# Kernel tuning notes

Hardware: AMD Instinct MI355X
Metric: run time of the kernel (lower is better)

Reference implementation:

```python
import jax, jax.numpy as jnp
import numpy as np

NEG_SLOPE = 0.01  # nn.LeakyReLU default


def setup_inputs() -> dict:
    key = jax.random.key(0)
    k1, k2, k3, k4, k5, k6 = jax.random.split(key, 6)
    N, E, F_IN, F_OUT = 50000, 800000, 256, 64
    x = jax.random.normal(k1, (N, F_IN), dtype=jnp.float32)
    src = jax.random.randint(k2, (E,), 0, N, dtype=jnp.int32)
    dst = jax.random.randint(k3, (E,), 0, N, dtype=jnp.int32)
    # nn.init.normal_(weight, 0, 0.5) for both Linear layers (no bias)
    W1 = 0.5 * jax.random.normal(k4, (F_OUT, F_IN), dtype=jnp.float32)
    W2 = 0.5 * jax.random.normal(k5, (F_OUT, F_OUT), dtype=jnp.float32)
    # detGAT.a = torch.rand(2*out_feats, 1)
    a = jax.random.uniform(k6, (2 * F_OUT, 1), dtype=jnp.float32)
    return {"x": x, "W1": W1, "W2": W2, "a": a, "src": src, "dst": dst}


def reference(x, W1, W2, a, src, dst):
    N, d = x.shape[0], W1.shape[0]
    # model_base: linear -> (dropout, identity in eval) -> relu, twice
    z = jax.nn.relu(x @ W1.T)
    h = jax.nn.relu(z @ W2.T)  # [N, d]
    # detGAT edge score: LeakyReLU(concat([h_dst, h_src]) @ a)
    # split a so we compute per-node dot products once instead of an [E, 2d] concat
    a_dst, a_src = a[:d, 0], a[d:, 0]
    s_dst = h @ a_dst  # [N]
    s_src = h @ a_src  # [N]
    score = jax.nn.leaky_relu(s_dst[dst] + s_src[src], NEG_SLOPE)  # [E]
    # edge_softmax: softmax over incoming edges of each destination node
    m = jax.ops.segment_max(score, dst, num_segments=N)  # [N]
    e = jnp.exp(score - m[dst])
    ssum = jax.ops.segment_sum(e, dst, num_segments=N)  # [N]
    w = e / ssum[dst]  # [E]
    # weighted scatter-sum of src features to dst nodes
    res = jax.ops.segment_sum(h[src] * w[:, None], dst, num_segments=N)  # [N, d]
    return jax.nn.relu(h - res)
```

## Files before the change

kernel.cpp:

```cpp
#include <hip/hip_runtime.h>
#include <math.h>

#define F_IN 256
#define F_OUT 64
#define NEG_SLOPE 0.01f
#define CAP 8192
#define NB2 256

typedef unsigned short ushort8_t __attribute__((ext_vector_type(8)));
typedef __bf16 bf16x8 __attribute__((ext_vector_type(8)));
typedef float f32x16 __attribute__((ext_vector_type(16)));

__device__ inline unsigned short f2bf(float f) {
    unsigned u = __float_as_uint(f);
    u += 0x7FFF + ((u >> 16) & 1);
    return (unsigned short)(u >> 16);
}
__device__ inline float bf2f(unsigned short u) {
    return __uint_as_float(((unsigned)u) << 16);
}
__device__ inline void splitbf(float x, unsigned short& hi, unsigned short& lo) {
    hi = f2bf(x);
    lo = f2bf(x - bf2f(hi));
}
__device__ inline bf16x8 asbf8(ushort8_t u) {
    union { ushort8_t u; bf16x8 b; } c; c.u = u; return c.b;
}
__device__ inline void split8(const float4& p0, const float4& p1, bf16x8& ah, bf16x8& al) {
    ushort8_t h, l;
    unsigned short th, tl;
    splitbf(p0.x, th, tl); h[0] = th; l[0] = tl;
    splitbf(p0.y, th, tl); h[1] = th; l[1] = tl;
    splitbf(p0.z, th, tl); h[2] = th; l[2] = tl;
    splitbf(p0.w, th, tl); h[3] = th; l[3] = tl;
    splitbf(p1.x, th, tl); h[4] = th; l[4] = tl;
    splitbf(p1.y, th, tl); h[5] = th; l[5] = tl;
    splitbf(p1.z, th, tl); h[6] = th; l[6] = tl;
    splitbf(p1.w, th, tl); h[7] = th; l[7] = tl;
    ah = asbf8(h); al = asbf8(l);
}
__device__ inline float redq32(float v) {
    v += __shfl_xor(v, 1);  v += __shfl_xor(v, 2);  v += __shfl_xor(v, 4);
    v += __shfl_xor(v, 8);  v += __shfl_xor(v, 16);
    return v;
}

__global__ __launch_bounds__(256)
void prep_frag_kernel(const float* __restrict__ W1, const float* __restrict__ W2,
                      unsigned short* __restrict__ w1fh, unsigned short* __restrict__ w1fl,
                      unsigned short* __restrict__ w2fh, unsigned short* __restrict__ w2fl)
{
    int idx = blockIdx.x * blockDim.x + threadIdx.x;
    int jj = idx & 7, l = (idx >> 3) & 63, t = idx >> 9;
    {
        int nt = t & 1, gks = t >> 1;
        int f = nt * 32 + (l & 31);
        int k = gks * 16 + (l >> 5) * 8 + jj;
        unsigned short hi, lo;
        splitbf(W1[f * F_IN + k], hi, lo);
        w1fh[idx] = hi; w1fl[idx] = lo;
    }
    if (idx < 4096) {
        int nt = t & 1, ks = t >> 1;
        int f = nt * 32 + (l & 31);
        int j = ks * 16 + (l >> 5) * 8 + jj;
        unsigned short hi, lo;
        splitbf(W2[f * F_OUT + j], hi, lo);
        w2fh[idx] = hi; w2fl[idx] = lo;
    }
}

__global__ __launch_bounds__(128, 2)
void mlp_kernel(const float* __restrict__ x,
                const unsigned short* __restrict__ w1fh,
                const unsigned short* __restrict__ w1fl,
                const unsigned short* __restrict__ w2fh,
                const unsigned short* __restrict__ w2fl,
                const float* __restrict__ a,
                unsigned short* __restrict__ hb,
                float* __restrict__ sdst,
                float* __restrict__ ssrc, int N)
{
    __shared__ __align__(16) unsigned short zbuf[2 * 4224];

    const int tid = threadIdx.x;
    const int lane = tid & 63;
    const int w = __builtin_amdgcn_readfirstlane(tid >> 6);
    const int ml = lane & 31;
    const int q = lane >> 5;
    const int node0w = blockIdx.x * 64 + w * 32;

    unsigned short* zh = zbuf + w * 4224;
    unsigned short* zl = zh + 2112;

    const int rowc = min(node0w + ml, N - 1);
    const float* __restrict__ xrow = x + (size_t)rowc * F_IN + q * 8;

    f32x16 acc0, acc1;
#pragma unroll
    for (int i = 0; i < 16; i++) { acc0[i] = 0.f; acc1[i] = 0.f; }

    float4 p0 = *(const float4*)(xrow);
    float4 p1 = *(const float4*)(xrow + 4);
    ushort8_t b0h = *(const ushort8_t*)(w1fh + (lane) * 8);
    ushort8_t b0l = *(const ushort8_t*)(w1fl + (lane) * 8);
    ushort8_t b1h = *(const ushort8_t*)(w1fh + (64 + lane) * 8);
    ushort8_t b1l = *(const ushort8_t*)(w1fl + (64 + lane) * 8);

#pragma unroll
    for (int gks = 0; gks < 16; gks++) {
        const int nx = gks < 15 ? gks + 1 : 15;
        float4 q0 = *(const float4*)(xrow + nx * 16);
        float4 q1 = *(const float4*)(xrow + nx * 16 + 4);
        ushort8_t c0h = *(const ushort8_t*)(w1fh + ((nx * 2 + 0) * 64 + lane) * 8);
        ushort8_t c0l = *(const ushort8_t*)(w1fl + ((nx * 2 + 0) * 64 + lane) * 8);
        ushort8_t c1h = *(const ushort8_t*)(w1fh + ((nx * 2 + 1) * 64 + lane) * 8);
        ushort8_t c1l = *(const ushort8_t*)(w1fl + ((nx * 2 + 1) * 64 + lane) * 8);

        bf16x8 ah, al;
        split8(p0, p1, ah, al);
        acc0 = __builtin_amdgcn_mfma_f32_32x32x16_bf16(ah, asbf8(b0h), acc0, 0, 0, 0);
        acc0 = __builtin_amdgcn_mfma_f32_32x32x16_bf16(ah, asbf8(b0l), acc0, 0, 0, 0);
        acc0 = __builtin_amdgcn_mfma_f32_32x32x16_bf16(al, asbf8(b0h), acc0, 0, 0, 0);
        acc1 = __builtin_amdgcn_mfma_f32_32x32x16_bf16(ah, asbf8(b1h), acc1, 0, 0, 0);
        acc1 = __builtin_amdgcn_mfma_f32_32x32x16_bf16(ah, asbf8(b1l), acc1, 0, 0, 0);
        acc1 = __builtin_amdgcn_mfma_f32_32x32x16_bf16(al, asbf8(b1h), acc1, 0, 0, 0);

        p0 = q0; p1 = q1;
        b0h = c0h; b0l = c0l; b1h = c1h; b1l = c1l;
    }

#pragma unroll
    for (int reg = 0; reg < 16; reg++) {
        int nd = (reg & 3) + 8 * (reg >> 2) + 4 * q;
        float z0 = fmaxf(acc0[reg], 0.f);
        float z1 = fmaxf(acc1[reg], 0.f);
        unsigned short h_, l_;
        splitbf(z0, h_, l_);
        zh[nd * 66 + ml] = h_; zl[nd * 66 + ml] = l_;
        splitbf(z1, h_, l_);
        zh[nd * 66 + 32 + ml] = h_; zl[nd * 66 + 32 + ml] = l_;
    }

    f32x16 hacc0, hacc1;
#pragma unroll
    for (int i = 0; i < 16; i++) { hacc0[i] = 0.f; hacc1[i] = 0.f; }
#pragma unroll
    for (int ks = 0; ks < 4; ks++) {
        ushort8_t wh0 = *(const ushort8_t*)(w2fh + ((ks * 2 + 0) * 64 + lane) * 8);
        ushort8_t wl0 = *(const ushort8_t*)(w2fl + ((ks * 2 + 0) * 64 + lane) * 8);
        ushort8_t wh1 = *(const ushort8_t*)(w2fh + ((ks * 2 + 1) * 64 + lane) * 8);
        ushort8_t wl1 = *(const ushort8_t*)(w2fl + ((ks * 2 + 1) * 64 + lane) * 8);
        bf16x8 ah = asbf8(*(const ushort8_t*)(zh + ml * 66 + ks * 16 + q * 8));
        bf16x8 al = asbf8(*(const ushort8_t*)(zl + ml * 66 + ks * 16 + q * 8));
        hacc0 = __builtin_amdgcn_mfma_f32_32x32x16_bf16(ah, asbf8(wh0), hacc0, 0, 0, 0);
        hacc0 = __builtin_amdgcn_mfma_f32_32x32x16_bf16(ah, asbf8(wl0), hacc0, 0, 0, 0);
        hacc0 = __builtin_amdgcn_mfma_f32_32x32x16_bf16(al, asbf8(wh0), hacc0, 0, 0, 0);
        hacc1 = __builtin_amdgcn_mfma_f32_32x32x16_bf16(ah, asbf8(wh1), hacc1, 0, 0, 0);
        hacc1 = __builtin_amdgcn_mfma_f32_32x32x16_bf16(ah, asbf8(wl1), hacc1, 0, 0, 0);
        hacc1 = __builtin_amdgcn_mfma_f32_32x32x16_bf16(al, asbf8(wh1), hacc1, 0, 0, 0);
    }

    const float aD0 = a[ml],            aD1 = a[32 + ml];
    const float aS0 = a[F_OUT + ml],    aS1 = a[F_OUT + 32 + ml];

    float sdv = 0.f, ssv = 0.f;
#pragma unroll
    for (int reg = 0; reg < 16; reg++) {
        int nd = (reg & 3) + 8 * (reg >> 2) + 4 * q;
        float h0 = fmaxf(hacc0[reg], 0.f);
        float h1 = fmaxf(hacc1[reg], 0.f);
        float td = redq32(h0 * aD0 + h1 * aD1);
        float ts = redq32(h0 * aS0 + h1 * aS1);
        if (ml == nd) { sdv = td; ssv = ts; }
        int gn = node0w + nd;
        if (gn < N) {
            hb[(size_t)gn * F_OUT + ml]      = f2bf(h0);
            hb[(size_t)gn * F_OUT + 32 + ml] = f2bf(h1);
        }
    }
    {
        int gn = node0w + ml;
        if ((((ml >> 2) & 1) == q) && gn < N) {
            sdst[gn] = sdv;
            ssrc[gn] = ssv;
        }
    }
}

__global__ __launch_bounds__(1024)
void scatter_fused_kernel(const int* __restrict__ src, const int* __restrict__ dst,
                          int* __restrict__ cursor, int* __restrict__ edata,
                          int E, int chunk)
{
    __shared__ int lh[256], lbase[256], lcur[256];
    const int tid = threadIdx.x;
    if (tid < 256) lh[tid] = 0;
    __syncthreads();
    const int beg = blockIdx.x * chunk;
    const int end = min(E, beg + chunk);
    for (int i = beg + tid; i < end; i += 1024)
        atomicAdd(&lh[((unsigned)dst[i]) >> 8], 1);
    __syncthreads();
    if (tid < 256) {
        int c = lh[tid];
        lbase[tid] = c ? atomicAdd(&cursor[tid], c) : 0;
        lcur[tid] = 0;
    }
    __syncthreads();
    for (int i = beg + tid; i < end; i += 1024) {
        int d = dst[i];
        int s = src[i];
        int b = ((unsigned)d) >> 8;
        int rk = atomicAdd(&lcur[b], 1);
        edata[b * CAP + lbase[b] + rk] = ((d & 0xFF) << 16) | s;
    }
}

__global__ __launch_bounds__(1024)
void bucket_sort_kernel(const int* __restrict__ cursor,
                        const int* __restrict__ edata,
                        int* __restrict__ ssorted,
                        int* __restrict__ cnt, int* __restrict__ offs, int N)
{
    __shared__ int hist[256];
    __shared__ int excl[256];
    const int tid = threadIdx.x;
    const int lane = tid & 63;
    const int cb = blockIdx.x;
    const int base = cb * CAP;
    const int ecnt = cursor[cb];

    if (tid < 256) hist[tid] = 0;
    __syncthreads();
    for (int i = tid; i < ecnt; i += 1024)
        atomicAdd(&hist[((unsigned)edata[base + i]) >> 16], 1);
    __syncthreads();

    if (tid < 64) {
        int v0 = hist[lane * 4], v1 = hist[lane * 4 + 1];
        int v2 = hist[lane * 4 + 2], v3 = hist[lane * 4 + 3];
        int ts = v0 + v1 + v2 + v3;
        int s = ts;
#pragma unroll
        for (int d = 1; d < 64; d <<= 1) {
            int t = __shfl_up(s, d);
            if (lane >= d) s += t;
        }
        int e = s - ts;
        excl[lane * 4] = e;
        excl[lane * 4 + 1] = e + v0;
        excl[lane * 4 + 2] = e + v0 + v1;
        excl[lane * 4 + 3] = e + v0 + v1 + v2;
    }
    __syncthreads();

    if (tid < 256) {
        int d = cb * 256 + tid;
        if (d < N) {
            cnt[d] = hist[tid];
            offs[d] = base + excl[tid];
        }
    }
    __syncthreads();

    for (int i = tid; i < ecnt; i += 1024) {
        int pack = edata[base + i];
        int low = ((unsigned)pack) >> 16;
        int rk = atomicAdd(&excl[low], 1);
        ssorted[base + rk] = pack & 0xFFFF;
    }
}

__global__ __launch_bounds__(256)
void aggregate_kernel(const unsigned short* __restrict__ hb,
                      const float* __restrict__ sdst,
                      const float* __restrict__ ssrc,
                      const int* __restrict__ offs,
                      const int* __restrict__ cnt,
                      const int* __restrict__ ssorted,
                      float* __restrict__ out, int N)
{
    __shared__ float2 ws_sh[4][64];
    const int lane = threadIdx.x & 63;
    const int wid = threadIdx.x >> 6;
    const int d = blockIdx.x * 4 + wid;
    if (d >= N) return;

    const int off = offs[d];
    const int deg = cnt[d];
    const float sdd = sdst[d];
    float M = -INFINITY, S = 0.f, res = 0.f;

    for (int cb = 0; cb < deg; cb += 64) {
        int ce = min(64, deg - cb);
        float score = -INFINITY;
        int s = 0;
        if (lane < ce) {
            s = ssorted[off + cb + lane];
            float sc = sdd + ssrc[s];
            score = sc > 0.f ? sc : NEG_SLOPE * sc;
        }
        float mc = score;
#pragma unroll
        for (int dd = 32; dd > 0; dd >>= 1)
            mc = fmaxf(mc, __shfl_xor(mc, dd));
        float newM = fmaxf(M, mc);
        float scale = __expf(M - newM);
        float w = (lane < ce) ? __expf(score - newM) : 0.f;
        ws_sh[wid][lane] = make_float2(w, __int_as_float(s));
        float csum = w;
#pragma unroll
        for (int dd = 32; dd > 0; dd >>= 1)
            csum += __shfl_xor(csum, dd);
        S = S * scale + csum;
        __builtin_amdgcn_wave_barrier();

        float c[8];
#pragma unroll
        for (int i = 0; i < 8; i++) c[i] = 0.f;
        const int ceo = (ce + 7) & ~7;
        for (int e = 0; e < ceo; e += 8) {
#pragma unroll
            for (int i = 0; i < 8; i++) {
                float2 t = ws_sh[wid][e + i];
                int se = __builtin_amdgcn_readfirstlane(__float_as_int(t.y));
                c[i] = fmaf(t.x, bf2f(hb[((unsigned)se << 6) + lane]), c[i]);
            }
        }
        float t = ((c[0] + c[1]) + (c[2] + c[3])) + ((c[4] + c[5]) + (c[6] + c[7]));
        res = res * scale + t;
        __builtin_amdgcn_wave_barrier();
        M = newM;
    }

    float hf = bf2f(hb[((unsigned)d << 6) + lane]);
    float r = (S > 0.f) ? (hf - res / S) : hf;
    out[(size_t)d * F_OUT + lane] = r > 0.f ? r : 0.f;
}

extern "C" void kernel_launch(void* const* d_in, const int* in_sizes, int n_in,
                              void* d_out, int out_size, void* d_ws,
                              size_t ws_size, hipStream_t stream)
{
    const float* x  = (const float*)d_in[0];
    const float* W1 = (const float*)d_in[1];
    const float* W2 = (const float*)d_in[2];
    const float* a  = (const float*)d_in[3];
    const int* src  = (const int*)d_in[4];
    const int* dst  = (const int*)d_in[5];
    const int N = in_sizes[0] / F_IN;
    const int E = in_sizes[4];

    float* ws = (float*)d_ws;
    float* sdst = ws;
    float* ssrc = sdst + N;
    unsigned short* w1fh = (unsigned short*)(ssrc + N);
    unsigned short* w1fl = w1fh + 16384;
    unsigned short* w2fh = w1fl + 16384;
    unsigned short* w2fl = w2fh + 4096;
    unsigned short* hb = w2fl + 4096;
    int* cnt    = (int*)(hb + (size_t)N * F_OUT);
    int* offs   = cnt + N;
    int* cursor = offs + N;
    int* edata  = cursor + 256;
    int* ssorted = edata + 196 * CAP;

    const int nbc = (N + 255) >> 8;
    const int chunk = (E + NB2 - 1) / NB2;

    hipMemsetAsync(cursor, 0, 256 * sizeof(int), stream);
    prep_frag_kernel<<<64, 256, 0, stream>>>(W1, W2, w1fh, w1fl, w2fh, w2fl);
    mlp_kernel<<<(N + 63) / 64, 128, 0, stream>>>(x, w1fh, w1fl, w2fh, w2fl, a,
                                                  hb, sdst, ssrc, N);
    scatter_fused_kernel<<<NB2, 1024, 0, stream>>>(src, dst, cursor, edata, E, chunk);
    bucket_sort_kernel<<<nbc, 1024, 0, stream>>>(cursor, edata, ssorted, cnt, offs, N);
    aggregate_kernel<<<(N + 3) / 4, 256, 0, stream>>>(hb, sdst, ssrc, offs, cnt,
                                                      ssorted, (float*)d_out, N);
}
```

Measured before the change: 164.3 us.

## Merge independent stages into shared launches to cut kernel count

The weight-fragment prep now runs inside the edge-scatter kernel as 16 extra blocks, and the MLP and per-bucket sort run as disjoint block ranges of one launch. Five kernels become three, which removes launch gaps and lets the compute-heavy MLP overlap with the memory and atomic-bound sort. The MLP blocks grow to 256 threads (4 waves) so both roles share a block size, and the sort now runs with 256 threads instead of 1024. That lowers sort parallelism per bucket and raises LDS use per block, which may cut occupancy for the MLP part.

Result: faster. 152.9 us (-7.0%).

```diff
diff --git a/kernel.cpp b/kernel.cpp
--- a/kernel.cpp
+++ b/kernel.cpp
@@ -45,159 +45,43 @@
     return v;
 }
 
-__global__ __launch_bounds__(256)
-void prep_frag_kernel(const float* __restrict__ W1, const float* __restrict__ W2,
-                      unsigned short* __restrict__ w1fh, unsigned short* __restrict__ w1fl,
-                      unsigned short* __restrict__ w2fh, unsigned short* __restrict__ w2fl)
-{
-    int idx = blockIdx.x * blockDim.x + threadIdx.x;
-    int jj = idx & 7, l = (idx >> 3) & 63, t = idx >> 9;
-    {
-        int nt = t & 1, gks = t >> 1;
-        int f = nt * 32 + (l & 31);
-        int k = gks * 16 + (l >> 5) * 8 + jj;
-        unsigned short hi, lo;
-        splitbf(W1[f * F_IN + k], hi, lo);
-        w1fh[idx] = hi; w1fl[idx] = lo;
-    }
-    if (idx < 4096) {
-        int nt = t & 1, ks = t >> 1;
-        int f = nt * 32 + (l & 31);
-        int j = ks * 16 + (l >> 5) * 8 + jj;
-        unsigned short hi, lo;
-        splitbf(W2[f * F_OUT + j], hi, lo);
-        w2fh[idx] = hi; w2fl[idx] = lo;
-    }
-}
-
-__global__ __launch_bounds__(128, 2)
-void mlp_kernel(const float* __restrict__ x,
-                const unsigned short* __restrict__ w1fh,
-                const unsigned short* __restrict__ w1fl,
-                const unsigned short* __restrict__ w2fh,
-                const unsigned short* __restrict__ w2fl,
-                const float* __restrict__ a,
-                unsigned short* __restrict__ hb,
-                float* __restrict__ sdst,
-                float* __restrict__ ssrc, int N)
-{
-    __shared__ __align__(16) unsigned short zbuf[2 * 4224];
-
-    const int tid = threadIdx.x;
-    const int lane = tid & 63;
-    const int w = __builtin_amdgcn_readfirstlane(tid >> 6);
-    const int ml = lane & 31;
-    const int q = lane >> 5;
-    const int node0w = blockIdx.x * 64 + w * 32;
-
-    unsigned short* zh = zbuf + w * 4224;
-    unsigned short* zl = zh + 2112;
-
-    const int rowc = min(node0w + ml, N - 1);
-    const float* __restrict__ xrow = x + (size_t)rowc * F_IN + q * 8;
-
-    f32x16 acc0, acc1;
-#pragma unroll
-    for (int i = 0; i < 16; i++) { acc0[i] = 0.f; acc1[i] = 0.f; }
-
-    float4 p0 = *(const float4*)(xrow);
-    float4 p1 = *(const float4*)(xrow + 4);
-    ushort8_t b0h = *(const ushort8_t*)(w1fh + (lane) * 8);
-    ushort8_t b0l = *(const ushort8_t*)(w1fl + (lane) * 8);
-    ushort8_t b1h = *(const ushort8_t*)(w1fh + (64 + lane) * 8);
-    ushort8_t b1l = *(const ushort8_t*)(w1fl + (64 + lane) * 8);
-
-#pragma unroll
-    for (int gks = 0; gks < 16; gks++) {
-        const int nx = gks < 15 ? gks + 1 : 15;
-        float4 q0 = *(const float4*)(xrow + nx * 16);
-        float4 q1 = *(const float4*)(xrow + nx * 16 + 4);
-        ushort8_t c0h = *(const ushort8_t*)(w1fh + ((nx * 2 + 0) * 64 + lane) * 8);
-        ushort8_t c0l = *(const ushort8_t*)(w1fl + ((nx * 2 + 0) * 64 + lane) * 8);
-        ushort8_t c1h = *(const ushort8_t*)(w1fh + ((nx * 2 + 1) * 64 + lane) * 8);
-        ushort8_t c1l = *(const ushort8_t*)(w1fl + ((nx * 2 + 1) * 64 + lane) * 8);
-
-        bf16x8 ah, al;
-        split8(p0, p1, ah, al);
-        acc0 = __builtin_amdgcn_mfma_f32_32x32x16_bf16(ah, asbf8(b0h), acc0, 0, 0, 0);
-        acc0 = __builtin_amdgcn_mfma_f32_32x32x16_bf16(ah, asbf8(b0l), acc0, 0, 0, 0);
-        acc0 = __builtin_amdgcn_mfma_f32_32x32x16_bf16(al, asbf8(b0h), acc0, 0, 0, 0);
-        acc1 = __builtin_amdgcn_mfma_f32_32x32x16_bf16(ah, asbf8(b1h), acc1, 0, 0, 0);
-        acc1 = __builtin_amdgcn_mfma_f32_32x32x16_bf16(ah, asbf8(b1l), acc1, 0, 0, 0);
-        acc1 = __builtin_amdgcn_mfma_f32_32x32x16_bf16(al, asbf8(b1h), acc1, 0, 0, 0);
-
-        p0 = q0; p1 = q1;
-        b0h = c0h; b0l = c0l; b1h = c1h; b1l = c1l;
-    }
-
-#pragma unroll
-    for (int reg = 0; reg < 16; reg++) {
-        int nd = (reg & 3) + 8 * (reg >> 2) + 4 * q;
-        float z0 = fmaxf(acc0[reg], 0.f);
-        float z1 = fmaxf(acc1[reg], 0.f);
-        unsigned short h_, l_;
-        splitbf(z0, h_, l_);
-        zh[nd * 66 + ml] = h_; zl[nd * 66 + ml] = l_;
-        splitbf(z1, h_, l_);
-        zh[nd * 66 + 32 + ml] = h_; zl[nd * 66 + 32 + ml] = l_;
-    }
-
-    f32x16 hacc0, hacc1;
-#pragma unroll
-    for (int i = 0; i < 16; i++) { hacc0[i] = 0.f; hacc1[i] = 0.f; }
-#pragma unroll
-    for (int ks = 0; ks < 4; ks++) {
-        ushort8_t wh0 = *(const ushort8_t*)(w2fh + ((ks * 2 + 0) * 64 + lane) * 8);
-        ushort8_t wl0 = *(const ushort8_t*)(w2fl + ((ks * 2 + 0) * 64 + lane) * 8);
-        ushort8_t wh1 = *(const ushort8_t*)(w2fh + ((ks * 2 + 1) * 64 + lane) * 8);
-        ushort8_t wl1 = *(const ushort8_t*)(w2fl + ((ks * 2 + 1) * 64 + lane) * 8);
-        bf16x8 ah = asbf8(*(const ushort8_t*)(zh + ml * 66 + ks * 16 + q * 8));
-        bf16x8 al = asbf8(*(const ushort8_t*)(zl + ml * 66 + ks * 16 + q * 8));
-        hacc0 = __builtin_amdgcn_mfma_f32_32x32x16_bf16(ah, asbf8(wh0), hacc0, 0, 0, 0);
-        hacc0 = __builtin_amdgcn_mfma_f32_32x32x16_bf16(ah, asbf8(wl0), hacc0, 0, 0, 0);
-        hacc0 = __builtin_amdgcn_mfma_f32_32x32x16_bf16(al, asbf8(wh0), hacc0, 0, 0, 0);
-        hacc1 = __builtin_amdgcn_mfma_f32_32x32x16_bf16(ah, asbf8(wh1), hacc1, 0, 0, 0);
-        hacc1 = __builtin_amdgcn_mfma_f32_32x32x16_bf16(ah, asbf8(wl1), hacc1, 0, 0, 0);
-        hacc1 = __builtin_amdgcn_mfma_f32_32x32x16_bf16(al, asbf8(wh1), hacc1, 0, 0, 0);
-    }
-
-    const float aD0 = a[ml],            aD1 = a[32 + ml];
-    const float aS0 = a[F_OUT + ml],    aS1 = a[F_OUT + 32 + ml];
-
-    float sdv = 0.f, ssv = 0.f;
-#pragma unroll
-    for (int reg = 0; reg < 16; reg++) {
-        int nd = (reg & 3) + 8 * (reg >> 2) + 4 * q;
-        float h0 = fmaxf(hacc0[reg], 0.f);
-        float h1 = fmaxf(hacc1[reg], 0.f);
-        float td = redq32(h0 * aD0 + h1 * aD1);
-        float ts = redq32(h0 * aS0 + h1 * aS1);
-        if (ml == nd) { sdv = td; ssv = ts; }
-        int gn = node0w + nd;
-        if (gn < N) {
-            hb[(size_t)gn * F_OUT + ml]      = f2bf(h0);
-            hb[(size_t)gn * F_OUT + 32 + ml] = f2bf(h1);
-        }
-    }
-    {
-        int gn = node0w + ml;
-        if ((((ml >> 2) & 1) == q) && gn < N) {
-            sdst[gn] = sdv;
-            ssrc[gn] = ssv;
-        }
-    }
-}
-
 __global__ __launch_bounds__(1024)
-void scatter_fused_kernel(const int* __restrict__ src, const int* __restrict__ dst,
-                          int* __restrict__ cursor, int* __restrict__ edata,
-                          int E, int chunk)
+void prep_scatter_kernel(const float* __restrict__ W1, const float* __restrict__ W2,
+                         unsigned short* __restrict__ w1fh, unsigned short* __restrict__ w1fl,
+                         unsigned short* __restrict__ w2fh, unsigned short* __restrict__ w2fl,
+                         const int* __restrict__ src, const int* __restrict__ dst,
+                         int* __restrict__ cursor, int* __restrict__ edata,
+                         int E, int chunk)
 {
     __shared__ int lh[256], lbase[256], lcur[256];
     const int tid = threadIdx.x;
+
+    if (blockIdx.x < 16) {
+        int idx = blockIdx.x * 1024 + tid;
+        int jj = idx & 7, l = (idx >> 3) & 63, t = idx >> 9;
+        {
+            int nt = t & 1, gks = t >> 1;
+            int f = nt * 32 + (l & 31);
+            int k = gks * 16 + (l >> 5) * 8 + jj;
+            unsigned short hi, lo;
+            splitbf(W1[f * F_IN + k], hi, lo);
+            w1fh[idx] = hi; w1fl[idx] = lo;
+        }
+        if (idx < 4096) {
+            int nt = t & 1, ks = t >> 1;
+            int f = nt * 32 + (l & 31);
+            int j = ks * 16 + (l >> 5) * 8 + jj;
+            unsigned short hi, lo;
+            splitbf(W2[f * F_OUT + j], hi, lo);
+            w2fh[idx] = hi; w2fl[idx] = lo;
+        }
+        return;
+    }
+
+    const int bid = blockIdx.x - 16;
     if (tid < 256) lh[tid] = 0;
     __syncthreads();
-    const int beg = blockIdx.x * chunk;
+    const int beg = bid * chunk;
     const int end = min(E, beg + chunk);
     for (int i = beg + tid; i < end; i += 1024)
         atomicAdd(&lh[((unsigned)dst[i]) >> 8], 1);
@@ -217,23 +101,141 @@
     }
 }
 
-__global__ __launch_bounds__(1024)
-void bucket_sort_kernel(const int* __restrict__ cursor,
-                        const int* __restrict__ edata,
-                        int* __restrict__ ssorted,
-                        int* __restrict__ cnt, int* __restrict__ offs, int N)
+__global__ __launch_bounds__(256)
+void mlp_sort_kernel(const float* __restrict__ x,
+                     const unsigned short* __restrict__ w1fh,
+                     const unsigned short* __restrict__ w1fl,
+                     const unsigned short* __restrict__ w2fh,
+                     const unsigned short* __restrict__ w2fl,
+                     const float* __restrict__ a,
+                     unsigned short* __restrict__ hb,
+                     float* __restrict__ sdst,
+                     float* __restrict__ ssrc, int N,
+                     const int* __restrict__ cursor,
+                     const int* __restrict__ edata,
+                     int* __restrict__ ssorted,
+                     int* __restrict__ cnt, int* __restrict__ offs,
+                     int MLPB)
 {
+    __shared__ __align__(16) unsigned short zbuf[4 * 4224];
     __shared__ int hist[256];
     __shared__ int excl[256];
+
     const int tid = threadIdx.x;
     const int lane = tid & 63;
-    const int cb = blockIdx.x;
+
+    if (blockIdx.x < MLPB) {
+        const int wid = __builtin_amdgcn_readfirstlane(tid >> 6);
+        const int ml = lane & 31;
+        const int q = lane >> 5;
+        const int node0w = blockIdx.x * 128 + wid * 32;
+
+        unsigned short* zh = zbuf + wid * 4224;
+        unsigned short* zl = zh + 2112;
+
+        const int rowc = min(node0w + ml, N - 1);
+        const float* __restrict__ xrow = x + (size_t)rowc * F_IN + q * 8;
+
+        f32x16 acc0, acc1;
+#pragma unroll
+        for (int i = 0; i < 16; i++) { acc0[i] = 0.f; acc1[i] = 0.f; }
+
+        float4 p0 = *(const float4*)(xrow);
+        float4 p1 = *(const float4*)(xrow + 4);
+        ushort8_t b0h = *(const ushort8_t*)(w1fh + (lane) * 8);
+        ushort8_t b0l = *(const ushort8_t*)(w1fl + (lane) * 8);
+        ushort8_t b1h = *(const ushort8_t*)(w1fh + (64 + lane) * 8);
+        ushort8_t b1l = *(const ushort8_t*)(w1fl + (64 + lane) * 8);
+
+#pragma unroll
+        for (int gks = 0; gks < 16; gks++) {
+            const int nx = gks < 15 ? gks + 1 : 15;
+            float4 q0 = *(const float4*)(xrow + nx * 16);
+            float4 q1 = *(const float4*)(xrow + nx * 16 + 4);
+            ushort8_t c0h = *(const ushort8_t*)(w1fh + ((nx * 2 + 0) * 64 + lane) * 8);
+            ushort8_t c0l = *(const ushort8_t*)(w1fl + ((nx * 2 + 0) * 64 + lane) * 8);
+            ushort8_t c1h = *(const ushort8_t*)(w1fh + ((nx * 2 + 1) * 64 + lane) * 8);
+            ushort8_t c1l = *(const ushort8_t*)(w1fl + ((nx * 2 + 1) * 64 + lane) * 8);
+
+            bf16x8 ah, al;
+            split8(p0, p1, ah, al);
+            acc0 = __builtin_amdgcn_mfma_f32_32x32x16_bf16(ah, asbf8(b0h), acc0, 0, 0, 0);
+            acc0 = __builtin_amdgcn_mfma_f32_32x32x16_bf16(ah, asbf8(b0l), acc0, 0, 0, 0);
+            acc0 = __builtin_amdgcn_mfma_f32_32x32x16_bf16(al, asbf8(b0h), acc0, 0, 0, 0);
+            acc1 = __builtin_amdgcn_mfma_f32_32x32x16_bf16(ah, asbf8(b1h), acc1, 0, 0, 0);
+            acc1 = __builtin_amdgcn_mfma_f32_32x32x16_bf16(ah, asbf8(b1l), acc1, 0, 0, 0);
+            acc1 = __builtin_amdgcn_mfma_f32_32x32x16_bf16(al, asbf8(b1h), acc1, 0, 0, 0);
+
+            p0 = q0; p1 = q1;
+            b0h = c0h; b0l = c0l; b1h = c1h; b1l = c1l;
+        }
+
+#pragma unroll
+        for (int reg = 0; reg < 16; reg++) {
+            int nd = (reg & 3) + 8 * (reg >> 2) + 4 * q;
+            float z0 = fmaxf(acc0[reg], 0.f);
+            float z1 = fmaxf(acc1[reg], 0.f);
+            unsigned short h_, l_;
+            splitbf(z0, h_, l_);
+            zh[nd * 66 + ml] = h_; zl[nd * 66 + ml] = l_;
+            splitbf(z1, h_, l_);
+            zh[nd * 66 + 32 + ml] = h_; zl[nd * 66 + 32 + ml] = l_;
+        }
+
+        f32x16 hacc0, hacc1;
+#pragma unroll
+        for (int i = 0; i < 16; i++) { hacc0[i] = 0.f; hacc1[i] = 0.f; }
+#pragma unroll
+        for (int ks = 0; ks < 4; ks++) {
+            ushort8_t wh0 = *(const ushort8_t*)(w2fh + ((ks * 2 + 0) * 64 + lane) * 8);
+            ushort8_t wl0 = *(const ushort8_t*)(w2fl + ((ks * 2 + 0) * 64 + lane) * 8);
+            ushort8_t wh1 = *(const ushort8_t*)(w2fh + ((ks * 2 + 1) * 64 + lane) * 8);
+            ushort8_t wl1 = *(const ushort8_t*)(w2fl + ((ks * 2 + 1) * 64 + lane) * 8);
+            bf16x8 ah = asbf8(*(const ushort8_t*)(zh + ml * 66 + ks * 16 + q * 8));
+            bf16x8 al = asbf8(*(const ushort8_t*)(zl + ml * 66 + ks * 16 + q * 8));
+            hacc0 = __builtin_amdgcn_mfma_f32_32x32x16_bf16(ah, asbf8(wh0), hacc0, 0, 0, 0);
+            hacc0 = __builtin_amdgcn_mfma_f32_32x32x16_bf16(ah, asbf8(wl0), hacc0, 0, 0, 0);
+            hacc0 = __builtin_amdgcn_mfma_f32_32x32x16_bf16(al, asbf8(wh0), hacc0, 0, 0, 0);
+            hacc1 = __builtin_amdgcn_mfma_f32_32x32x16_bf16(ah, asbf8(wh1), hacc1, 0, 0, 0);
+            hacc1 = __builtin_amdgcn_mfma_f32_32x32x16_bf16(ah, asbf8(wl1), hacc1, 0, 0, 0);
+            hacc1 = __builtin_amdgcn_mfma_f32_32x32x16_bf16(al, asbf8(wh1), hacc1, 0, 0, 0);
+        }
+
+        const float aD0 = a[ml],            aD1 = a[32 + ml];
+        const float aS0 = a[F_OUT + ml],    aS1 = a[F_OUT + 32 + ml];
+
+        float sdv = 0.f, ssv = 0.f;
+#pragma unroll
+        for (int reg = 0; reg < 16; reg++) {
+            int nd = (reg & 3) + 8 * (reg >> 2) + 4 * q;
+            float h0 = fmaxf(hacc0[reg], 0.f);
+            float h1 = fmaxf(hacc1[reg], 0.f);
+            float td = redq32(h0 * aD0 + h1 * aD1);
+            float ts = redq32(h0 * aS0 + h1 * aS1);
+            if (ml == nd) { sdv = td; ssv = ts; }
+            int gn = node0w + nd;
+            if (gn < N) {
+                hb[(size_t)gn * F_OUT + ml]      = f2bf(h0);
+                hb[(size_t)gn * F_OUT + 32 + ml] = f2bf(h1);
+            }
+        }
+        {
+            int gn = node0w + ml;
+            if ((((ml >> 2) & 1) == q) && gn < N) {
+                sdst[gn] = sdv;
+                ssrc[gn] = ssv;
+            }
+        }
+        return;
+    }
+
+    const int cb = blockIdx.x - MLPB;
     const int base = cb * CAP;
     const int ecnt = cursor[cb];
 
-    if (tid < 256) hist[tid] = 0;
-    __syncthreads();
-    for (int i = tid; i < ecnt; i += 1024)
+    hist[tid] = 0;
+    __syncthreads();
+    for (int i = tid; i < ecnt; i += 256)
         atomicAdd(&hist[((unsigned)edata[base + i]) >> 16], 1);
     __syncthreads();
 
@@ -255,7 +257,7 @@
     }
     __syncthreads();
 
-    if (tid < 256) {
+    {
         int d = cb * 256 + tid;
         if (d < N) {
             cnt[d] = hist[tid];
@@ -264,7 +266,7 @@
     }
     __syncthreads();
 
-    for (int i = tid; i < ecnt; i += 1024) {
+    for (int i = tid; i < ecnt; i += 256) {
         int pack = edata[base + i];
         int low = ((unsigned)pack) >> 16;
         int rk = atomicAdd(&excl[low], 1);
@@ -367,14 +369,16 @@
     int* ssorted = edata + 196 * CAP;
 
     const int nbc = (N + 255) >> 8;
+    const int MLPB = (N + 127) >> 7;
     const int chunk = (E + NB2 - 1) / NB2;
 
     hipMemsetAsync(cursor, 0, 256 * sizeof(int), stream);
-    prep_frag_kernel<<<64, 256, 0, stream>>>(W1, W2, w1fh, w1fl, w2fh, w2fl);
-    mlp_kernel<<<(N + 63) / 64, 128, 0, stream>>>(x, w1fh, w1fl, w2fh, w2fl, a,
-                                                  hb, sdst, ssrc, N);
-    scatter_fused_kernel<<<NB2, 1024, 0, stream>>>(src, dst, cursor, edata, E, chunk);
-    bucket_sort_kernel<<<nbc, 1024, 0, stream>>>(cursor, edata, ssorted, cnt, offs, N);
+    prep_scatter_kernel<<<16 + NB2, 1024, 0, stream>>>(W1, W2, w1fh, w1fl, w2fh, w2fl,
+                                                       src, dst, cursor, edata, E, chunk);
+    mlp_sort_kernel<<<MLPB + nbc, 256, 0, stream>>>(x, w1fh, w1fl, w2fh, w2fl, a,
+                                                    hb, sdst, ssrc, N,
+                                                    cursor, edata, ssorted, cnt, offs,
+                                                    MLPB);
     aggregate_kernel<<<(N + 3) / 4, 256, 0, stream>>>(hb, sdst, ssrc, offs, cnt,
                                                       ssorted, (float*)d_out, N);
 }
```
